# Optimization experiments

Measured on AMD Instinct MI355X. Metric: run time of the kernel, lower is better.

## Reference

```python
import jax, jax.numpy as jnp
import numpy as np

NUM_SEGMENTS = 2048  # matches fill_max of superpixels_results


def setup_inputs() -> dict:
    key = jax.random.key(0)
    k1, k2 = jax.random.split(key)
    B, C, H, W = 2, 64, 1024, 1024
    superpixels_results = jax.random.randint(k1, (B, H, W), 0, NUM_SEGMENTS, dtype=jnp.int32)
    feats = jax.random.normal(k2, (B, C, H, W), dtype=jnp.float32)
    return {"superpixels_results": superpixels_results, "feats": feats}


def reference(superpixels_results, feats):
    # Faithful to the original torch code: `return` sits inside the batch loop,
    # so ONLY batch 0 is processed, and c counts unique ids of batch 0 only.
    C = feats.shape[1]
    sp = superpixels_results[0].reshape(-1)            # [P] int segment ids
    x = feats[0].reshape(C, -1).T                      # [P, C]

    seg_sum = jax.ops.segment_sum(x, sp, num_segments=NUM_SEGMENTS)        # [S, C]
    seg_sumsq = jax.ops.segment_sum(x * x, sp, num_segments=NUM_SEGMENTS)  # [S, C]
    counts = jax.ops.segment_sum(jnp.ones_like(sp, dtype=x.dtype), sp,
                                 num_segments=NUM_SEGMENTS)                # [S]

    n = jnp.maximum(counts, 1.0)[:, None]              # avoid div-by-zero
    # sum over pixels of (x - mean)^2, per segment and channel:
    var_sum = seg_sumsq - seg_sum * seg_sum / n        # [S, C]
    # original does var_loss_t.mean() over [C, n] elements:
    per_seg = var_sum.sum(axis=1) / (C * jnp.maximum(counts, 1.0))  # [S]

    valid = counts >= 2.0                              # segments with <2 px skipped
    var_loss = jnp.where(valid, per_seg, 0.0).sum()
    c = (counts > 0.0).sum().astype(x.dtype)           # unique ids in batch 0
    return var_loss / c
```

## Files before the change

kernel.cpp:

```cpp
#include <hip/hip_runtime.h>

#define S_SEG 2048
#define C_ALL 64
#define P_PIX (1024 * 1024)
#define CH_PER 4
#define N_GROUPS 16
#define N_CHUNKS 64
#define BLOCK 512
#define PIX_PER_BLOCK (P_PIX / N_CHUNKS)

#define OFF_SQ   131072
#define OFF_CNT  133120
#define OFF_ACC  135168
#define N_ZERO   135170

__global__ void zero_kernel(float* __restrict__ p, int n) {
    int i = blockIdx.x * blockDim.x + threadIdx.x;
    if (i < n) p[i] = 0.0f;
}

__global__ __launch_bounds__(256) void count_kernel(const int* __restrict__ sp,
                                                    float* __restrict__ cnt_g) {
    __shared__ float cnt_h[S_SEG];
    const int tid = threadIdx.x;
    for (int i = tid; i < S_SEG; i += 256) cnt_h[i] = 0.0f;
    __syncthreads();
    const int base = blockIdx.x * (P_PIX / 32);
    const int4* sp4 = (const int4*)(sp + base);
    const int iters = (P_PIX / 32) / (256 * 4);
    for (int it = 0; it < iters; ++it) {
        const int4 s4 = sp4[it * 256 + tid];
        atomicAdd(&cnt_h[s4.x], 1.0f);
        atomicAdd(&cnt_h[s4.y], 1.0f);
        atomicAdd(&cnt_h[s4.z], 1.0f);
        atomicAdd(&cnt_h[s4.w], 1.0f);
    }
    __syncthreads();
    for (int i = tid; i < S_SEG; i += 256) {
        const float v = cnt_h[i];
        if (v != 0.0f) unsafeAtomicAdd(&cnt_g[i], v);
    }
}

__global__ __launch_bounds__(BLOCK) void accum_kernel(
        const int* __restrict__ sp, const float* __restrict__ feats,
        float* __restrict__ sum_g, float* __restrict__ sq_g) {
    __shared__ float hist[CH_PER * S_SEG];
    __shared__ float sq_h[S_SEG];
    const int tid = threadIdx.x;
    const int chunk = blockIdx.x;
    const int grp = blockIdx.y;
    const int c0 = grp * CH_PER;

    for (int i = tid; i < CH_PER * S_SEG; i += BLOCK) hist[i] = 0.0f;
    for (int i = tid; i < S_SEG; i += BLOCK) sq_h[i] = 0.0f;
    __syncthreads();

    const int base = chunk * PIX_PER_BLOCK;
    const int4* sp4 = (const int4*)(sp + base);
    const int iters = PIX_PER_BLOCK / (BLOCK * 4);

    for (int it = 0; it < iters; ++it) {
        const int idx = it * BLOCK + tid;
        const int4 s4 = sp4[idx];
        float sq0 = 0.f, sq1 = 0.f, sq2 = 0.f, sq3 = 0.f;
#pragma unroll
        for (int c = 0; c < CH_PER; ++c) {
            const float4 v =
                ((const float4*)(feats + (size_t)(c0 + c) * P_PIX + base))[idx];
            atomicAdd(&hist[c * S_SEG + s4.x], v.x); sq0 = fmaf(v.x, v.x, sq0);
            atomicAdd(&hist[c * S_SEG + s4.y], v.y); sq1 = fmaf(v.y, v.y, sq1);
            atomicAdd(&hist[c * S_SEG + s4.z], v.z); sq2 = fmaf(v.z, v.z, sq2);
            atomicAdd(&hist[c * S_SEG + s4.w], v.w); sq3 = fmaf(v.w, v.w, sq3);
        }
        atomicAdd(&sq_h[s4.x], sq0);
        atomicAdd(&sq_h[s4.y], sq1);
        atomicAdd(&sq_h[s4.z], sq2);
        atomicAdd(&sq_h[s4.w], sq3);
    }
    __syncthreads();

    for (int i = tid; i < CH_PER * S_SEG; i += BLOCK) {
        const int c = i >> 11, s = i & (S_SEG - 1);
        const float v = hist[i];
        if (v != 0.0f) unsafeAtomicAdd(&sum_g[(size_t)(c0 + c) * S_SEG + s], v);
    }
    for (int i = tid; i < S_SEG; i += BLOCK) {
        const float v = sq_h[i];
        if (v != 0.0f) unsafeAtomicAdd(&sq_g[i], v);
    }
}

__global__ void finalize_kernel(const float* __restrict__ sum_g,
                                const float* __restrict__ sq_g,
                                const float* __restrict__ cnt_g,
                                float* __restrict__ accum) {
    const int s = blockIdx.x * blockDim.x + threadIdx.x;
    const float cnt = cnt_g[s];
    const float n = fmaxf(cnt, 1.0f);
    float acc = 0.0f;
#pragma unroll 8
    for (int c = 0; c < C_ALL; ++c) {
        const float v = sum_g[c * S_SEG + s];
        acc = fmaf(v, v, acc);
    }
    const float var = sq_g[s] - acc / n;
    const float per = var / (64.0f * n);
    float loss = (cnt >= 2.0f) ? per : 0.0f;
    float cc = (cnt > 0.0f) ? 1.0f : 0.0f;
    for (int off = 32; off; off >>= 1) {
        loss += __shfl_down(loss, off);
        cc += __shfl_down(cc, off);
    }
    if ((threadIdx.x & 63) == 0) {
        unsafeAtomicAdd(&accum[0], loss);
        unsafeAtomicAdd(&accum[1], cc);
    }
}

__global__ void final_div(const float* __restrict__ accum, float* __restrict__ out) {
    out[0] = accum[0] / accum[1];
}

extern "C" void kernel_launch(void* const* d_in, const int* in_sizes, int n_in,
                              void* d_out, int out_size, void* d_ws, size_t ws_size,
                              hipStream_t stream) {
    const int* sp = (const int*)d_in[0];
    const float* feats = (const float*)d_in[1];
    float* ws = (float*)d_ws;
    float* sum_g = ws;
    float* sq_g = ws + OFF_SQ;
    float* cnt_g = ws + OFF_CNT;
    float* accum = ws + OFF_ACC;

    zero_kernel<<<(N_ZERO + 255) / 256, 256, 0, stream>>>(ws, N_ZERO);

    count_kernel<<<32, 256, 0, stream>>>(sp, cnt_g);

    dim3 grid(N_CHUNKS, N_GROUPS);
    accum_kernel<<<grid, BLOCK, 0, stream>>>(sp, feats, sum_g, sq_g);

    finalize_kernel<<<S_SEG / 256, 256, 0, stream>>>(sum_g, sq_g, cnt_g, accum);
    final_div<<<1, 1, 0, stream>>>(accum, (float*)d_out);
}
```

Before: 1.000 ms.

## Use int counts, widen count grid, single-block finalize, unsafe LDS atomics

Segment counts become integer atomics, and the count kernel runs on 256 blocks instead of 32. The finalize and final-divide kernels merge into one 1024-thread block that reduces through shared memory and writes the output directly, which removes one launch and the global accumulator atomics. The shared-memory histogram atomics in the main accumulation loop switch to unsafeAtomicAdd, which may compile to native LDS float add instead of a CAS loop. In exchange, the finalize step now runs on a single block.

```diff
diff --git a/kernel.cpp b/kernel.cpp
--- a/kernel.cpp
+++ b/kernel.cpp
@@ -11,8 +11,7 @@
 
 #define OFF_SQ   131072
 #define OFF_CNT  133120
-#define OFF_ACC  135168
-#define N_ZERO   135170
+#define N_ZERO   135168
 
 __global__ void zero_kernel(float* __restrict__ p, int n) {
     int i = blockIdx.x * blockDim.x + threadIdx.x;
@@ -20,25 +19,25 @@
 }
 
 __global__ __launch_bounds__(256) void count_kernel(const int* __restrict__ sp,
-                                                    float* __restrict__ cnt_g) {
-    __shared__ float cnt_h[S_SEG];
+                                                    int* __restrict__ cnt_g) {
+    __shared__ int cnt_h[S_SEG];
     const int tid = threadIdx.x;
-    for (int i = tid; i < S_SEG; i += 256) cnt_h[i] = 0.0f;
+    for (int i = tid; i < S_SEG; i += 256) cnt_h[i] = 0;
     __syncthreads();
-    const int base = blockIdx.x * (P_PIX / 32);
+    const int base = blockIdx.x * (P_PIX / 256);
     const int4* sp4 = (const int4*)(sp + base);
-    const int iters = (P_PIX / 32) / (256 * 4);
+    const int iters = (P_PIX / 256) / (256 * 4);
     for (int it = 0; it < iters; ++it) {
         const int4 s4 = sp4[it * 256 + tid];
-        atomicAdd(&cnt_h[s4.x], 1.0f);
-        atomicAdd(&cnt_h[s4.y], 1.0f);
-        atomicAdd(&cnt_h[s4.z], 1.0f);
-        atomicAdd(&cnt_h[s4.w], 1.0f);
+        atomicAdd(&cnt_h[s4.x], 1);
+        atomicAdd(&cnt_h[s4.y], 1);
+        atomicAdd(&cnt_h[s4.z], 1);
+        atomicAdd(&cnt_h[s4.w], 1);
     }
     __syncthreads();
     for (int i = tid; i < S_SEG; i += 256) {
-        const float v = cnt_h[i];
-        if (v != 0.0f) unsafeAtomicAdd(&cnt_g[i], v);
+        const int v = cnt_h[i];
+        if (v != 0) atomicAdd(&cnt_g[i], v);
     }
 }
 
@@ -68,15 +67,15 @@
         for (int c = 0; c < CH_PER; ++c) {
             const float4 v =
                 ((const float4*)(feats + (size_t)(c0 + c) * P_PIX + base))[idx];
-            atomicAdd(&hist[c * S_SEG + s4.x], v.x); sq0 = fmaf(v.x, v.x, sq0);
-            atomicAdd(&hist[c * S_SEG + s4.y], v.y); sq1 = fmaf(v.y, v.y, sq1);
-            atomicAdd(&hist[c * S_SEG + s4.z], v.z); sq2 = fmaf(v.z, v.z, sq2);
-            atomicAdd(&hist[c * S_SEG + s4.w], v.w); sq3 = fmaf(v.w, v.w, sq3);
+            unsafeAtomicAdd(&hist[c * S_SEG + s4.x], v.x); sq0 = fmaf(v.x, v.x, sq0);
+            unsafeAtomicAdd(&hist[c * S_SEG + s4.y], v.y); sq1 = fmaf(v.y, v.y, sq1);
+            unsafeAtomicAdd(&hist[c * S_SEG + s4.z], v.z); sq2 = fmaf(v.z, v.z, sq2);
+            unsafeAtomicAdd(&hist[c * S_SEG + s4.w], v.w); sq3 = fmaf(v.w, v.w, sq3);
         }
-        atomicAdd(&sq_h[s4.x], sq0);
-        atomicAdd(&sq_h[s4.y], sq1);
-        atomicAdd(&sq_h[s4.z], sq2);
-        atomicAdd(&sq_h[s4.w], sq3);
+        unsafeAtomicAdd(&sq_h[s4.x], sq0);
+        unsafeAtomicAdd(&sq_h[s4.y], sq1);
+        unsafeAtomicAdd(&sq_h[s4.z], sq2);
+        unsafeAtomicAdd(&sq_h[s4.w], sq3);
     }
     __syncthreads();
 
@@ -91,35 +90,42 @@
     }
 }
 
-__global__ void finalize_kernel(const float* __restrict__ sum_g,
-                                const float* __restrict__ sq_g,
-                                const float* __restrict__ cnt_g,
-                                float* __restrict__ accum) {
-    const int s = blockIdx.x * blockDim.x + threadIdx.x;
-    const float cnt = cnt_g[s];
-    const float n = fmaxf(cnt, 1.0f);
-    float acc = 0.0f;
+__global__ __launch_bounds__(1024) void finalize_kernel(
+        const float* __restrict__ sum_g, const float* __restrict__ sq_g,
+        const int* __restrict__ cnt_g, float* __restrict__ out) {
+    __shared__ float red_l[16], red_c[16];
+    const int tid = threadIdx.x;
+    float loss = 0.0f, cc = 0.0f;
+#pragma unroll
+    for (int k = 0; k < 2; ++k) {
+        const int s = tid + k * 1024;
+        const float cnt = (float)cnt_g[s];
+        const float n = fmaxf(cnt, 1.0f);
+        float acc = 0.0f;
 #pragma unroll 8
-    for (int c = 0; c < C_ALL; ++c) {
-        const float v = sum_g[c * S_SEG + s];
-        acc = fmaf(v, v, acc);
+        for (int c = 0; c < C_ALL; ++c) {
+            const float v = sum_g[c * S_SEG + s];
+            acc = fmaf(v, v, acc);
+        }
+        const float var = sq_g[s] - acc / n;
+        loss += (cnt >= 2.0f) ? var / (64.0f * n) : 0.0f;
+        cc += (cnt > 0.0f) ? 1.0f : 0.0f;
     }
-    const float var = sq_g[s] - acc / n;
-    const float per = var / (64.0f * n);
-    float loss = (cnt >= 2.0f) ? per : 0.0f;
-    float cc = (cnt > 0.0f) ? 1.0f : 0.0f;
     for (int off = 32; off; off >>= 1) {
         loss += __shfl_down(loss, off);
         cc += __shfl_down(cc, off);
     }
-    if ((threadIdx.x & 63) == 0) {
-        unsafeAtomicAdd(&accum[0], loss);
-        unsafeAtomicAdd(&accum[1], cc);
+    const int wave = tid >> 6;
+    if ((tid & 63) == 0) { red_l[wave] = loss; red_c[wave] = cc; }
+    __syncthreads();
+    if (tid < 16) {
+        loss = red_l[tid]; cc = red_c[tid];
+        for (int off = 8; off; off >>= 1) {
+            loss += __shfl_down(loss, off);
+            cc += __shfl_down(cc, off);
+        }
+        if (tid == 0) out[0] = loss / cc;
     }
-}
-
-__global__ void final_div(const float* __restrict__ accum, float* __restrict__ out) {
-    out[0] = accum[0] / accum[1];
 }
 
 extern "C" void kernel_launch(void* const* d_in, const int* in_sizes, int n_in,
@@ -130,16 +136,14 @@
     float* ws = (float*)d_ws;
     float* sum_g = ws;
     float* sq_g = ws + OFF_SQ;
-    float* cnt_g = ws + OFF_CNT;
-    float* accum = ws + OFF_ACC;
+    int* cnt_g = (int*)(ws + OFF_CNT);
 
     zero_kernel<<<(N_ZERO + 255) / 256, 256, 0, stream>>>(ws, N_ZERO);
 
-    count_kernel<<<32, 256, 0, stream>>>(sp, cnt_g);
+    count_kernel<<<256, 256, 0, stream>>>(sp, cnt_g);
 
     dim3 grid(N_CHUNKS, N_GROUPS);
     accum_kernel<<<grid, BLOCK, 0, stream>>>(sp, feats, sum_g, sq_g);
 
-    finalize_kernel<<<S_SEG / 256, 256, 0, stream>>>(sum_g, sq_g, cnt_g, accum);
-    final_div<<<1, 1, 0, stream>>>(accum, (float*)d_out);
+    finalize_kernel<<<1, 1024, 0, stream>>>(sum_g, sq_g, cnt_g, (float*)d_out);
 }
```

Result: faster. 970.4 us (-3.0%).
